# Kernel tuning notes

Measured on AMD Instinct MI355X. Metric: run time of the kernel, lower is better.

The kernel has to match this reference:

```python
import jax, jax.numpy as jnp
import numpy as np

P, B, H, IN, L = 64, 256, 512, 2, 2


def setup_inputs() -> dict:
    key = jax.random.key(0)
    ks = jax.random.split(key, 16)
    s = 1.0 / np.sqrt(H)
    inp = {
        'input_traces': jax.random.normal(ks[0], (B, P, IN), jnp.float32),
        'h0': jax.random.normal(ks[1], (P, L, B, H), jnp.float32) * 0.1,
        'c0': jax.random.normal(ks[2], (P, L, B, H), jnp.float32) * 0.1,
        # layer 0 LSTM params (PyTorch layout: [4H, in] with gate order i,f,g,o)
        'w_ih0': jax.random.uniform(ks[3], (4 * H, IN), jnp.float32, -s, s),
        'w_hh0': jax.random.uniform(ks[4], (4 * H, H), jnp.float32, -s, s),
        'b_ih0': jax.random.uniform(ks[5], (4 * H,), jnp.float32, -s, s),
        'b_hh0': jax.random.uniform(ks[6], (4 * H,), jnp.float32, -s, s),
        # layer 1 LSTM params
        'w_ih1': jax.random.uniform(ks[7], (4 * H, H), jnp.float32, -s, s),
        'w_hh1': jax.random.uniform(ks[8], (4 * H, H), jnp.float32, -s, s),
        'b_ih1': jax.random.uniform(ks[9], (4 * H,), jnp.float32, -s, s),
        'b_hh1': jax.random.uniform(ks[10], (4 * H,), jnp.float32, -s, s),
    }
    return inp


def _lstm_forward(input_traces, h0, c0, params):
    # Fuse pedestrian and batch dims into one big batch PB = P*B; the original
    # loops over pedestrians calling the SAME LSTM weights, so this is exact.
    x = jnp.transpose(input_traces, (1, 0, 2)).reshape(P * B, IN)  # [PB, 2]
    h = jnp.transpose(h0, (1, 0, 2, 3)).reshape(L, P * B, H)       # [L, PB, H]
    c = jnp.transpose(c0, (1, 0, 2, 3)).reshape(L, P * B, H)
    h_next, c_next = [], []
    for l in range(L):
        wi, wh, bi, bh = params[l]
        gates = x @ wi.T + bi + h[l] @ wh.T + bh                   # [PB, 4H]
        ig, fg, gg, og = jnp.split(gates, 4, axis=-1)
        ig, fg, og = jax.nn.sigmoid(ig), jax.nn.sigmoid(fg), jax.nn.sigmoid(og)
        gg = jnp.tanh(gg)
        c_new = fg * c[l] + ig * gg
        h_new = og * jnp.tanh(c_new)
        h_next.append(h_new)
        c_next.append(c_new)
        x = h_new
    out = x.reshape(P, B, H).transpose(1, 0, 2)                    # [B, P, H]
    hn = jnp.stack(h_next).reshape(L, P, B, H).transpose(1, 0, 2, 3)
    cn = jnp.stack(c_next).reshape(L, P, B, H).transpose(1, 0, 2, 3)
    return out, hn, cn


def reference(input_traces, h0, c0, w_ih0, w_hh0, b_ih0, b_hh0,
              w_ih1, w_hh1, b_ih1, b_hh1):
    params = [(w_ih0, w_hh0, b_ih0, b_hh0), (w_ih1, w_hh1, b_ih1, b_hh1)]
    return _lstm_forward(input_traces, h0, c0, params)
```

## Files before the change

kernel.cpp:

```cpp
#include <hip/hip_runtime.h>
#include <hip/hip_bf16.h>

#define PP 64
#define BB 256
#define HH 512
#define MM (PP * BB)

#define HN_BASE (BB * PP * HH)
#define CN_BASE (HN_BASE + PP * 2 * BB * HH)

#define TILE8K 8192
#define WS_A0   0ull
#define WS_A1A  16777216ull
#define WS_A1B  33554432ull
#define WS_W0   50331648ull
#define WS_W1A  52428800ull
#define WS_W1B  54525952ull
#define WS_NEED 56623104ull

typedef __attribute__((ext_vector_type(8))) short bf16x8;
typedef __attribute__((ext_vector_type(4))) float floatx4;

__device__ __forceinline__ float sigf(float x) { return 1.0f / (1.0f + __expf(-x)); }
__device__ __forceinline__ float tanh_(float x) { return 2.0f / (1.0f + __expf(-2.0f * x)) - 1.0f; }

__device__ __forceinline__ short f2bf(float f) {
  unsigned u = __float_as_uint(f);
  u = (u + 0x7FFFu + ((u >> 16) & 1u)) >> 16;
  return (short)u;
}

template <typename T>
__device__ __forceinline__ float tofl(T v);
template <> __device__ __forceinline__ float tofl<float>(float v) { return v; }
template <> __device__ __forceinline__ float tofl<__hip_bfloat16>(__hip_bfloat16 v) { return __bfloat162float(v); }

template <typename T>
__device__ __forceinline__ T fromfl(float v);
template <> __device__ __forceinline__ float fromfl<float>(float v) { return v; }
template <> __device__ __forceinline__ __hip_bfloat16 fromfl<__hip_bfloat16>(float v) { return __float2bfloat16(v); }

template <typename T>
__device__ __forceinline__ bf16x8 load8(const T* p);
template <> __device__ __forceinline__ bf16x8 load8<__hip_bfloat16>(const __hip_bfloat16* p) {
  return *(const bf16x8*)p;
}
template <> __device__ __forceinline__ bf16x8 load8<float>(const float* p) {
  float4 f0 = *(const float4*)p;
  float4 f1 = *((const float4*)p + 1);
  bf16x8 v;
  v[0] = f2bf(f0.x); v[1] = f2bf(f0.y); v[2] = f2bf(f0.z); v[3] = f2bf(f0.w);
  v[4] = f2bf(f1.x); v[5] = f2bf(f1.y); v[6] = f2bf(f1.z); v[7] = f2bf(f1.w);
  return v;
}

__device__ __forceinline__ bool detect_f32(const void* w_ih0) {
  const unsigned short* p = (const unsigned short*)w_ih0;
  int l = threadIdx.x & 63;
  unsigned short a = p[2 * l], b = p[2 * l + 1];
  int big = ((a & 0x7F80) >= 0x3F80) || ((b & 0x7F80) >= 0x3F80);
  return __any(big);
}

__device__ __forceinline__ void gload16(void* ldsp, const void* g) {
  __builtin_amdgcn_global_load_lds(
      (const __attribute__((address_space(1))) unsigned int*)g,
      (__attribute__((address_space(3))) unsigned int*)ldsp, 16, 0, 0);
}

template <typename T>
__device__ __forceinline__ void prep_panel_body(const T* __restrict__ src, char* __restrict__ dst,
                                                char* lds) {
  const int tid = threadIdx.x;
  for (int cc = 0; cc < 8; ++cc) {
#pragma unroll
    for (int i = 0; i < 8; ++i) {
      int idx = i * 256 + tid;
      int row = idx >> 4;
      int c4  = idx & 15;
      int c   = c4 * 4;
      const T* p = src + (size_t)row * 512 + cc * 64 + c;
      short4 s;
      if constexpr (sizeof(T) == 4) {
        float4 f = *(const float4*)p;
        s.x = f2bf(f.x); s.y = f2bf(f.y); s.z = f2bf(f.z); s.w = f2bf(f.w);
      } else {
        s = *(const short4*)p;
      }
      int tile = c >> 5;
      int qd   = (c & 31) >> 3;
      int e0   = c & 7;
      int rb   = row >> 4, lr = row & 15;
      *(short4*)(lds + tile * 8192 + ((rb * 64 + qd * 16 + lr) * 16) + e0 * 2) = s;
    }
    __syncthreads();
#pragma unroll
    for (int i = 0; i < 4; ++i) {
      int idx = i * 256 + tid;
      int kt  = cc * 2 + (idx >> 9);
      *(bf16x8*)(dst + (size_t)kt * TILE8K + (size_t)(idx & 511) * 16) =
          *(const bf16x8*)(lds + (size_t)idx * 16);
    }
    __syncthreads();
  }
}

__global__ void __launch_bounds__(256)
prep_panel_k(const void* tensor, const void* det, void* ws,
             unsigned long long off0, unsigned long long off1, int is_hn) {
  const int pb = blockIdx.x, l = blockIdx.y;
  __shared__ __align__(16) char lds[16384];
  char* dst = (char*)ws + (l ? off1 : off0) + (size_t)pb * 16 * TILE8K;
  const size_t srcoff = (((size_t)(pb >> 1) * 2 + l) * 256 + (size_t)(pb & 1) * 128) * 512;
  if (detect_f32(det)) {
    const float* t = (const float*)tensor + (is_hn ? (size_t)HN_BASE : 0);
    prep_panel_body<float>(t + srcoff, dst, lds);
  } else {
    const __hip_bfloat16* t = (const __hip_bfloat16*)tensor + (is_hn ? (size_t)HN_BASE : 0);
    prep_panel_body<__hip_bfloat16>(t + srcoff, dst, lds);
  }
}

template <typename T>
__device__ __forceinline__ void prep_W_body(const T* __restrict__ w0, const T* __restrict__ w1a,
                                            const T* __restrict__ w1b, char* __restrict__ ws) {
  const int m = blockIdx.x >> 4, hb = blockIdx.x & 15, kt = blockIdx.y;
  const T* src = (m == 0) ? w0 : (m == 1 ? w1a : w1b);
  const size_t base = (m == 0) ? WS_W0 : (m == 1 ? WS_W1A : WS_W1B);
  char* dst = ws + base + ((size_t)(hb * 16 + kt)) * TILE8K;
  const int tid = threadIdx.x;
#pragma unroll
  for (int i = 0; i < 2; ++i) {
    int idx = i * 256 + tid;
    int ln  = idx & 63;
    int rb  = idx >> 6;
    int g   = rb >> 1, half = rb & 1;
    int j   = g * 512 + hb * 32 + half * 16 + (ln & 15);
    int col = kt * 32 + (ln >> 4) * 8;
    *(bf16x8*)(dst + (size_t)idx * 16) = load8<T>(src + (size_t)j * 512 + col);
  }
}

__global__ void __launch_bounds__(256) prep_W_k(const void* w0, const void* w1a, const void* w1b,
                                                const void* det, void* ws) {
  if (detect_f32(det)) prep_W_body<float>((const float*)w0, (const float*)w1a, (const float*)w1b, (char*)ws);
  else prep_W_body<__hip_bfloat16>((const __hip_bfloat16*)w0, (const __hip_bfloat16*)w1a,
                                   (const __hip_bfloat16*)w1b, (char*)ws);
}

template <typename T, int LAYER>
__device__ __forceinline__ void lstm_dma_body(
    const T* __restrict__ xin, const T* __restrict__ c0,
    const T* __restrict__ wih, const T* __restrict__ bih, const T* __restrict__ bhh,
    T* __restrict__ out, char* __restrict__ ws, char* lds)
{
  const int tid  = threadIdx.x;
  const int wg   = blockIdx.x;
  const int wgid = (wg & 7) * 256 + (wg >> 3);
  const int hb   = wgid & 15;
  const int nb   = wgid >> 4;
  const int lane = tid & 63;
  const int wid  = tid >> 6;
  const int quad = lane >> 4;
  const int lrow = lane & 15;
  const int p0   = nb >> 1;

  floatx4 acc[4][4];
#pragma unroll
  for (int g = 0; g < 4; ++g)
#pragma unroll
    for (int mi = 0; mi < 4; ++mi)
#pragma unroll
      for (int q = 0; q < 4; ++q) acc[g][mi][q] = 0.0f;

  const int a_rb0  = (wid >> 1) * 4;
  const int w_half = wid & 1;

  constexpr int KITERS = (LAYER == 0) ? 16 : 32;

  auto stage = [&](int buf, int kt) {
    const char *at, *wt;
    if (LAYER == 0) {
      at = ws + WS_A0  + ((size_t)(nb * 16 + kt)) * TILE8K;
      wt = ws + WS_W0  + ((size_t)(hb * 16 + kt)) * TILE8K;
    } else if (kt < 16) {
      at = ws + WS_A1A + ((size_t)(nb * 16 + kt)) * TILE8K;
      wt = ws + WS_W1A + ((size_t)(hb * 16 + kt)) * TILE8K;
    } else {
      at = ws + WS_A1B + ((size_t)(nb * 16 + kt - 16)) * TILE8K;
      wt = ws + WS_W1B + ((size_t)(hb * 16 + kt - 16)) * TILE8K;
    }
    char* la = lds + buf * 16384;
    char* lw = la + TILE8K;
#pragma unroll
    for (int i = 0; i < 2; ++i) {
      int base = (i * 4 + wid) * 1024;
      int off  = base + lane * 16;
      gload16(la + base, at + off);
      gload16(lw + base, wt + off);
    }
  };

  stage(0, 0);
  __syncthreads();

#pragma unroll
  for (int kt = 0; kt < KITERS; ++kt) {
    const int cur = kt & 1;
    if (kt + 1 < KITERS) stage(cur ^ 1, kt + 1);

    const char* la = lds + cur * 16384;
    const char* lw = la + TILE8K;
    bf16x8 aF[4], wF[4];
#pragma unroll
    for (int mi = 0; mi < 4; ++mi)
      aF[mi] = *(const bf16x8*)(la + ((a_rb0 + mi) * 1024) + lane * 16);
#pragma unroll
    for (int g = 0; g < 4; ++g)
      wF[g] = *(const bf16x8*)(lw + ((g * 2 + w_half) * 1024) + lane * 16);
#pragma unroll
    for (int g = 0; g < 4; ++g)
#pragma unroll
      for (int mi = 0; mi < 4; ++mi)
        acc[g][mi] = __builtin_amdgcn_mfma_f32_16x16x32_bf16(
            aF[mi], wF[g], acc[g][mi], 0, 0, 0);

    __syncthreads();
  }

  const int hloc = hb * 32 + w_half * 16 + lrow;
  float bias[4], wx0[4], wx1[4];
#pragma unroll
  for (int g = 0; g < 4; ++g) {
    int j = g * 512 + hloc;
    bias[g] = tofl<T>(bih[j]) + tofl<T>(bhh[j]);
    if (LAYER == 0) {
      wx0[g] = tofl<T>(wih[j * 2]);
      wx1[g] = tofl<T>(wih[j * 2 + 1]);
    }
  }
  const int crow0 = (p0 * 2 + LAYER) * 256;

#pragma unroll
  for (int mi = 0; mi < 4; ++mi) {
#pragma unroll
    for (int r = 0; r < 4; ++r) {
      int rr = (wid >> 1) * 64 + mi * 16 + quad * 4 + r;
      int b  = ((nb & 1) << 7) + rr;
      float gv0 = acc[0][mi][r] + bias[0];
      float gv1 = acc[1][mi][r] + bias[1];
      float gv2 = acc[2][mi][r] + bias[2];
      float gv3 = acc[3][mi][r] + bias[3];
      if (LAYER == 0) {
        float x0 = tofl<T>(xin[(b * 64 + p0) * 2]);
        float x1 = tofl<T>(xin[(b * 64 + p0) * 2 + 1]);
        gv0 += x0 * wx0[0] + x1 * wx1[0];
        gv1 += x0 * wx0[1] + x1 * wx1[1];
        gv2 += x0 * wx0[2] + x1 * wx1[2];
        gv3 += x0 * wx0[3] + x1 * wx1[3];
      }
      float ig = sigf(gv0), fg = sigf(gv1);
      float gg = tanh_(gv2), og = sigf(gv3);
      size_t ro = ((size_t)(crow0 + b)) * 512 + hloc;
      float co   = tofl<T>(c0[ro]);
      float cnew = fg * co + ig * gg;
      float hnew = og * tanh_(cnew);
      out[HN_BASE + ro] = fromfl<T>(hnew);
      out[CN_BASE + ro] = fromfl<T>(cnew);
      if (LAYER == 1)
        out[(size_t)(b * 64 + p0) * 512 + hloc] = fromfl<T>(hnew);
    }
  }
}

template <int LAYER>
__global__ void __launch_bounds__(256, 4)
lstm_dma(const void* xin, const void* c0, const void* wih,
         const void* bih, const void* bhh, const void* det,
         void* out, void* ws)
{
  __shared__ __align__(16) char lds[2 * 16384];
  if (detect_f32(det)) {
    lstm_dma_body<float, LAYER>((const float*)xin, (const float*)c0, (const float*)wih,
                                (const float*)bih, (const float*)bhh,
                                (float*)out, (char*)ws, lds);
  } else {
    lstm_dma_body<__hip_bfloat16, LAYER>((const __hip_bfloat16*)xin, (const __hip_bfloat16*)c0,
                                         (const __hip_bfloat16*)wih, (const __hip_bfloat16*)bih,
                                         (const __hip_bfloat16*)bhh,
                                         (__hip_bfloat16*)out, (char*)ws, lds);
  }
}

template <typename T, int LAYER>
__device__ __forceinline__ void lstm_body(
    const T* __restrict__ xin, const T* __restrict__ h0, const T* __restrict__ c0,
    const T* __restrict__ wih, const T* __restrict__ whh,
    const T* __restrict__ bih, const T* __restrict__ bhh,
    T* out, __hip_bfloat16* ldsA, __hip_bfloat16* ldsW)
{
  const int tid  = threadIdx.x;
  const int nb   = blockIdx.x;
  const int hb   = blockIdx.y;
  const int lane = tid & 63;
  const int wid  = tid >> 6;
  const int quad = lane >> 4;
  const int lrow = lane & 15;
  const int p0   = nb >> 1;

  floatx4 acc[4][4];
#pragma unroll
  for (int g = 0; g < 4; ++g)
#pragma unroll
    for (int mi = 0; mi < 4; ++mi)
#pragma unroll
      for (int q = 0; q < 4; ++q) acc[g][mi][q] = 0.0f;

  int arow[4], wrow[4];
#pragma unroll
  for (int mi = 0; mi < 4; ++mi) arow[mi] = (wid >> 1) * 64 + mi * 16 + lrow;
#pragma unroll
  for (int g = 0; g < 4; ++g) wrow[g] = g * 32 + (wid & 1) * 16 + lrow;

  const int sr = tid >> 3;
  const int sc = tid & 7;
  const int KITERS = (LAYER == 0) ? 8 : 16;

  for (int kt = 0; kt < KITERS; ++kt) {
    bf16x8 ra[4], rw[4];
#pragma unroll
    for (int round = 0; round < 4; ++round) {
      int r = sr + round * 32;
      int b = ((nb & 1) << 7) + r;
      const T* srcA;
      if (LAYER == 0) {
        srcA = h0 + ((size_t)((p0 * 2) * 256 + b)) * 512 + kt * 64 + sc * 8;
      } else {
        if (kt < 8)
          srcA = out + HN_BASE + ((size_t)((p0 * 2) * 256 + b)) * 512 + kt * 64 + sc * 8;
        else
          srcA = h0 + ((size_t)((p0 * 2 + 1) * 256 + b)) * 512 + (kt - 8) * 64 + sc * 8;
      }
      ra[round] = load8<T>(srcA);

      int j = (r >> 5) * 512 + hb * 32 + (r & 31);
      const T* srcW;
      if (LAYER == 0) {
        srcW = whh + (size_t)j * 512 + kt * 64 + sc * 8;
      } else {
        if (kt < 8) srcW = wih + (size_t)j * 512 + kt * 64 + sc * 8;
        else        srcW = whh + (size_t)j * 512 + (kt - 8) * 64 + sc * 8;
      }
      rw[round] = load8<T>(srcW);
    }

    __syncthreads();
#pragma unroll
    for (int round = 0; round < 4; ++round) {
      int r = sr + round * 32;
      int p = sc ^ (r & 7);
      *(bf16x8*)((char*)ldsA + r * 128 + p * 16) = ra[round];
      *(bf16x8*)((char*)ldsW + r * 128 + p * 16) = rw[round];
    }
    __syncthreads();

#pragma unroll
    for (int ks = 0; ks < 2; ++ks) {
      bf16x8 aF[4], wF[4];
#pragma unroll
      for (int mi = 0; mi < 4; ++mi) {
        int ch = (ks * 4 + quad) ^ (arow[mi] & 7);
        aF[mi] = *(const bf16x8*)((const char*)ldsA + arow[mi] * 128 + ch * 16);
      }
#pragma unroll
      for (int g = 0; g < 4; ++g) {
        int ch = (ks * 4 + quad) ^ (wrow[g] & 7);
        wF[g] = *(const bf16x8*)((const char*)ldsW + wrow[g] * 128 + ch * 16);
      }
#pragma unroll
      for (int g = 0; g < 4; ++g)
#pragma unroll
        for (int mi = 0; mi < 4; ++mi)
          acc[g][mi] = __builtin_amdgcn_mfma_f32_16x16x32_bf16(
              aF[mi], wF[g], acc[g][mi], 0, 0, 0);
    }
  }

  const int hloc = hb * 32 + (wid & 1) * 16 + lrow;
  float bias[4], wx0[4], wx1[4];
#pragma unroll
  for (int g = 0; g < 4; ++g) {
    int j = g * 512 + hloc;
    bias[g] = tofl<T>(bih[j]) + tofl<T>(bhh[j]);
    if (LAYER == 0) {
      wx0[g] = tofl<T>(wih[j * 2]);
      wx1[g] = tofl<T>(wih[j * 2 + 1]);
    }
  }
  const int crow0 = (p0 * 2 + LAYER) * 256;
#pragma unroll
  for (int mi = 0; mi < 4; ++mi) {
#pragma unroll
    for (int r = 0; r < 4; ++r) {
      int b = ((nb & 1) << 7) + (wid >> 1) * 64 + mi * 16 + quad * 4 + r;
      float gv0 = acc[0][mi][r] + bias[0];
      float gv1 = acc[1][mi][r] + bias[1];
      float gv2 = acc[2][mi][r] + bias[2];
      float gv3 = acc[3][mi][r] + bias[3];
      if (LAYER == 0) {
        float x0 = tofl<T>(xin[(b * 64 + p0) * 2]);
        float x1 = tofl<T>(xin[(b * 64 + p0) * 2 + 1]);
        gv0 += x0 * wx0[0] + x1 * wx1[0];
        gv1 += x0 * wx0[1] + x1 * wx1[1];
        gv2 += x0 * wx0[2] + x1 * wx1[2];
        gv3 += x0 * wx0[3] + x1 * wx1[3];
      }
      float ig = sigf(gv0), fg = sigf(gv1);
      float gg = tanh_(gv2), og = sigf(gv3);
      size_t ro = ((size_t)(crow0 + b)) * 512 + hloc;
      float co   = tofl<T>(c0[ro]);
      float cnew = fg * co + ig * gg;
      float hnew = og * tanh_(cnew);
      out[HN_BASE + ro] = fromfl<T>(hnew);
      out[CN_BASE + ro] = fromfl<T>(cnew);
      if (LAYER == 1)
        out[(size_t)(b * 64 + p0) * 512 + hloc] = fromfl<T>(hnew);
    }
  }
}

template <int LAYER>
__global__ void __launch_bounds__(256)
lstm_layer(const void* xin, const void* h0, const void* c0,
           const void* wih, const void* whh, const void* bih, const void* bhh,
           const void* w_ih0_detect, void* out)
{
  __shared__ __align__(16) __hip_bfloat16 ldsA[128 * 64];
  __shared__ __align__(16) __hip_bfloat16 ldsW[128 * 64];
  if (detect_f32(w_ih0_detect)) {
    lstm_body<float, LAYER>((const float*)xin, (const float*)h0, (const float*)c0,
                            (const float*)wih, (const float*)whh,
                            (const float*)bih, (const float*)bhh,
                            (float*)out, ldsA, ldsW);
  } else {
    lstm_body<__hip_bfloat16, LAYER>((const __hip_bfloat16*)xin, (const __hip_bfloat16*)h0,
                                     (const __hip_bfloat16*)c0, (const __hip_bfloat16*)wih,
                                     (const __hip_bfloat16*)whh, (const __hip_bfloat16*)bih,
                                     (const __hip_bfloat16*)bhh, (__hip_bfloat16*)out,
                                     ldsA, ldsW);
  }
}

extern "C" void kernel_launch(void* const* d_in, const int* in_sizes, int n_in,
                              void* d_out, int out_size, void* d_ws, size_t ws_size,
                              hipStream_t stream) {
  dim3 block(256);
  if (d_ws != nullptr && ws_size >= WS_NEED) {
    prep_panel_k<<<dim3(128, 2), block, 0, stream>>>(d_in[1], d_in[3], d_ws,
                                                     WS_A0, WS_A1B, 0);
    prep_W_k<<<dim3(48, 16), block, 0, stream>>>(d_in[4], d_in[7], d_in[8], d_in[3], d_ws);
    dim3 grid(2048);
    lstm_dma<0><<<grid, block, 0, stream>>>(d_in[0], d_in[2], d_in[3],
                                            d_in[5], d_in[6], d_in[3], d_out, d_ws);
    prep_panel_k<<<dim3(128, 1), block, 0, stream>>>(d_out, d_in[3], d_ws,
                                                     WS_A1A, WS_A1A, 1);
    lstm_dma<1><<<grid, block, 0, stream>>>(d_in[0], d_in[2], d_in[3],
                                            d_in[9], d_in[10], d_in[3], d_out, d_ws);
  } else {
    dim3 grid(MM / 128, HH / 32);
    lstm_layer<0><<<grid, block, 0, stream>>>(d_in[0], d_in[1], d_in[2],
                                              d_in[3], d_in[4], d_in[5], d_in[6],
                                              d_in[3], d_out);
    lstm_layer<1><<<grid, block, 0, stream>>>(d_in[0], d_in[1], d_in[2],
                                              d_in[7], d_in[8], d_in[9], d_in[10],
                                              d_in[3], d_out);
  }
}
```

Baseline: 483.2 us.

## Fuse layer-1 input panel packing into layer-0 epilogue and parallelize prep

Layer 0's epilogue now writes its new h values as bf16 into LDS in the packed MFMA tile layout and stores that tile straight to the workspace panel used by layer 1. This removes the separate prep_panel launch that re-read hn from the output and repacked it. The remaining prep_panel kernel now spreads its 8 column chunks across a grid dimension instead of looping inside each block. The lstm grid also drops the XCD-swizzled 1D block mapping for a plain 2D grid, which may change L2 locality on the multi-die GPU.

Measured after the change: 451.6 us. -6.5%, faster.

```diff
diff --git a/kernel.cpp b/kernel.cpp
--- a/kernel.cpp
+++ b/kernel.cpp
@@ -70,54 +70,48 @@
 
 template <typename T>
 __device__ __forceinline__ void prep_panel_body(const T* __restrict__ src, char* __restrict__ dst,
-                                                char* lds) {
+                                                char* lds, int cc) {
   const int tid = threadIdx.x;
-  for (int cc = 0; cc < 8; ++cc) {
-#pragma unroll
-    for (int i = 0; i < 8; ++i) {
-      int idx = i * 256 + tid;
-      int row = idx >> 4;
-      int c4  = idx & 15;
-      int c   = c4 * 4;
-      const T* p = src + (size_t)row * 512 + cc * 64 + c;
-      short4 s;
-      if constexpr (sizeof(T) == 4) {
-        float4 f = *(const float4*)p;
-        s.x = f2bf(f.x); s.y = f2bf(f.y); s.z = f2bf(f.z); s.w = f2bf(f.w);
-      } else {
-        s = *(const short4*)p;
-      }
-      int tile = c >> 5;
-      int qd   = (c & 31) >> 3;
-      int e0   = c & 7;
-      int rb   = row >> 4, lr = row & 15;
-      *(short4*)(lds + tile * 8192 + ((rb * 64 + qd * 16 + lr) * 16) + e0 * 2) = s;
-    }
-    __syncthreads();
-#pragma unroll
-    for (int i = 0; i < 4; ++i) {
-      int idx = i * 256 + tid;
-      int kt  = cc * 2 + (idx >> 9);
-      *(bf16x8*)(dst + (size_t)kt * TILE8K + (size_t)(idx & 511) * 16) =
-          *(const bf16x8*)(lds + (size_t)idx * 16);
-    }
-    __syncthreads();
+#pragma unroll
+  for (int i = 0; i < 8; ++i) {
+    int idx = i * 256 + tid;
+    int row = idx >> 4;
+    int c   = (idx & 15) * 4;
+    const T* p = src + (size_t)row * 512 + cc * 64 + c;
+    short4 s;
+    if constexpr (sizeof(T) == 4) {
+      float4 f = *(const float4*)p;
+      s.x = f2bf(f.x); s.y = f2bf(f.y); s.z = f2bf(f.z); s.w = f2bf(f.w);
+    } else {
+      s = *(const short4*)p;
+    }
+    int tile = c >> 5;
+    int qd   = (c & 31) >> 3;
+    int e0   = c & 7;
+    int rb   = row >> 4, lr = row & 15;
+    *(short4*)(lds + tile * 8192 + ((rb * 64 + qd * 16 + lr) * 16) + e0 * 2) = s;
+  }
+  __syncthreads();
+#pragma unroll
+  for (int i = 0; i < 4; ++i) {
+    int idx = i * 256 + tid;
+    int kt  = cc * 2 + (idx >> 9);
+    *(bf16x8*)(dst + (size_t)kt * TILE8K + (size_t)(idx & 511) * 16) =
+        *(const bf16x8*)(lds + (size_t)idx * 16);
   }
 }
 
 __global__ void __launch_bounds__(256)
 prep_panel_k(const void* tensor, const void* det, void* ws,
-             unsigned long long off0, unsigned long long off1, int is_hn) {
-  const int pb = blockIdx.x, l = blockIdx.y;
+             unsigned long long off0, unsigned long long off1) {
+  const int pb = blockIdx.x, cc = blockIdx.y, l = blockIdx.z;
   __shared__ __align__(16) char lds[16384];
   char* dst = (char*)ws + (l ? off1 : off0) + (size_t)pb * 16 * TILE8K;
   const size_t srcoff = (((size_t)(pb >> 1) * 2 + l) * 256 + (size_t)(pb & 1) * 128) * 512;
   if (detect_f32(det)) {
-    const float* t = (const float*)tensor + (is_hn ? (size_t)HN_BASE : 0);
-    prep_panel_body<float>(t + srcoff, dst, lds);
+    prep_panel_body<float>((const float*)tensor + srcoff, dst, lds, cc);
   } else {
-    const __hip_bfloat16* t = (const __hip_bfloat16*)tensor + (is_hn ? (size_t)HN_BASE : 0);
-    prep_panel_body<__hip_bfloat16>(t + srcoff, dst, lds);
+    prep_panel_body<__hip_bfloat16>((const __hip_bfloat16*)tensor + srcoff, dst, lds, cc);
   }
 }
 
@@ -155,10 +149,8 @@
     T* __restrict__ out, char* __restrict__ ws, char* lds)
 {
   const int tid  = threadIdx.x;
-  const int wg   = blockIdx.x;
-  const int wgid = (wg & 7) * 256 + (wg >> 3);
-  const int hb   = wgid & 15;
-  const int nb   = wgid >> 4;
+  const int hb   = blockIdx.x;
+  const int nb   = blockIdx.y;
   const int lane = tid & 63;
   const int wid  = tid >> 6;
   const int quad = lane >> 4;
@@ -240,6 +232,8 @@
     }
   }
   const int crow0 = (p0 * 2 + LAYER) * 256;
+  const int qd_h = (hloc >> 3) & 3;
+  const int el_h = hloc & 7;
 
 #pragma unroll
   for (int mi = 0; mi < 4; ++mi) {
@@ -267,8 +261,22 @@
       float hnew = og * tanh_(cnew);
       out[HN_BASE + ro] = fromfl<T>(hnew);
       out[CN_BASE + ro] = fromfl<T>(cnew);
+      if (LAYER == 0) {
+        int slot = ((rr >> 4) * 64) + qd_h * 16 + (rr & 15);
+        *(short*)(lds + slot * 16 + el_h * 2) = f2bf(hnew);
+      }
       if (LAYER == 1)
         out[(size_t)(b * 64 + p0) * 512 + hloc] = fromfl<T>(hnew);
+    }
+  }
+
+  if (LAYER == 0) {
+    __syncthreads();
+    char* a1a_tile = ws + WS_A1A + ((size_t)(nb * 16 + hb)) * TILE8K;
+#pragma unroll
+    for (int i = 0; i < 2; ++i) {
+      int idx = i * 256 + tid;
+      *(bf16x8*)(a1a_tile + (size_t)idx * 16) = *(const bf16x8*)(lds + (size_t)idx * 16);
     }
   }
 }
@@ -456,14 +464,12 @@
                               hipStream_t stream) {
   dim3 block(256);
   if (d_ws != nullptr && ws_size >= WS_NEED) {
-    prep_panel_k<<<dim3(128, 2), block, 0, stream>>>(d_in[1], d_in[3], d_ws,
-                                                     WS_A0, WS_A1B, 0);
+    prep_panel_k<<<dim3(128, 8, 2), block, 0, stream>>>(d_in[1], d_in[3], d_ws,
+                                                        WS_A0, WS_A1B);
     prep_W_k<<<dim3(48, 16), block, 0, stream>>>(d_in[4], d_in[7], d_in[8], d_in[3], d_ws);
-    dim3 grid(2048);
+    dim3 grid(HH / 32, MM / 128);
     lstm_dma<0><<<grid, block, 0, stream>>>(d_in[0], d_in[2], d_in[3],
                                             d_in[5], d_in[6], d_in[3], d_out, d_ws);
-    prep_panel_k<<<dim3(128, 1), block, 0, stream>>>(d_out, d_in[3], d_ws,
-                                                     WS_A1A, WS_A1A, 1);
     lstm_dma<1><<<grid, block, 0, stream>>>(d_in[0], d_in[2], d_in[3],
                                             d_in[9], d_in[10], d_in[3], d_out, d_ws);
   } else {
```
